# Optimization experiments

Measured on AMD Instinct MI355X. Metric: run time of the kernel, lower is better.

The kernel has to match this reference:

```python
import jax, jax.numpy as jnp
import numpy as np

B, S, D, E = 4, 4096, 1024, 8

def setup_inputs() -> dict:
    key = jax.random.key(0)
    k_h, k_wr, k_br, k_we = jax.random.split(key, 4)
    h = jax.random.normal(k_h, (B, S, D), dtype=jnp.float32)
    # route_weights: nn.Linear(D, E) -> weight [E, D], bias [E]
    W_route = jax.random.normal(k_wr, (E, D), dtype=jnp.float32) / np.sqrt(D)
    b_route = jax.random.normal(k_br, (E,), dtype=jnp.float32) * 0.01
    # edge_transforms: E x nn.Linear(D, D, bias=False) -> stacked [E, D_out, D_in]
    W_edges = jax.random.normal(k_we, (E, D, D), dtype=jnp.float32) / np.sqrt(D)
    layer_bias = jnp.zeros((D,), dtype=jnp.float32)
    return {"h": h, "W_route": W_route, "b_route": b_route,
            "W_edges": W_edges, "layer_bias": layer_bias}

def reference(h, W_route, b_route, W_edges, layer_bias):
    # route_logits = h @ W_route.T + b_route -> [B, S, E]
    route_logits = jnp.einsum('bsd,ed->bse', h, W_route) + b_route
    rw = jax.nn.softmax(route_logits, axis=-1)
    # fused: sum_e rw[b,s,e] * (h @ W_e.T) -> [B, S, D]
    out = jnp.einsum('bsd,efd,bse->bsf', h, W_edges, rw)
    out = out + layer_bias
    return jax.nn.gelu(out, approximate=False)  # torch F.gelu default is exact erf
```

## Files before the change

### kernel.cpp

```cpp
#include <hip/hip_runtime.h>
#include <hip/hip_bf16.h>

#define M_TOK 16384
#define DDIM  1024
#define NEXP  8
#define KP    (NEXP * DDIM)

typedef __bf16 bf16x8 __attribute__((ext_vector_type(8)));
typedef __bf16 bf16x4 __attribute__((ext_vector_type(4)));
typedef float  floatx4 __attribute__((ext_vector_type(4)));

__device__ __forceinline__ void gload_lds16(const void* g, void* l) {
    __builtin_amdgcn_global_load_lds(
        (__attribute__((address_space(1))) void*)(void*)g,
        (__attribute__((address_space(3))) void*)l,
        16, 0, 0);
}

#define CONV_BLOCKS  2048
#define ROUTE_BLOCKS 4096

__global__ __launch_bounds__(256) void prep_kernel(
    const float* __restrict__ h, const float* __restrict__ Wr,
    const float* __restrict__ br, const float* __restrict__ We,
    __bf16* __restrict__ hbf, float* __restrict__ rw, __bf16* __restrict__ Bp)
{
    __shared__ float Wrs[NEXP * DDIM];
    const int tid = threadIdx.x;

    if (blockIdx.x < CONV_BLOCKS) {
        size_t idx = ((size_t)blockIdx.x * 256 + tid) * 16;
        int e = (int)(idx >> 20);
        int f = (int)(idx >> 10) & 1023;
        int k = (int)idx & 1023;
        const float4* s4 = (const float4*)(We + idx);
        float a[16];
        #pragma unroll
        for (int i = 0; i < 4; ++i) {
            float4 v = s4[i];
            a[i*4+0] = v.x; a[i*4+1] = v.y; a[i*4+2] = v.z; a[i*4+3] = v.w;
        }
        bf16x8 o0, o1;
        #pragma unroll
        for (int i = 0; i < 8; ++i) { o0[i] = (__bf16)a[i]; o1[i] = (__bf16)a[8 + i]; }
        __bf16* d = Bp + (size_t)f * KP + (size_t)e * DDIM + k;
        *(bf16x8*)d       = o0;
        *(bf16x8*)(d + 8) = o1;
        return;
    }

    {
        const float4* s4 = (const float4*)Wr;
        float4* d4 = (float4*)Wrs;
        #pragma unroll
        for (int j = 0; j < 8; ++j) d4[j * 256 + tid] = s4[j * 256 + tid];
    }
    __syncthreads();

    const int wave = tid >> 6, lane = tid & 63;
    const int m = (blockIdx.x - CONV_BLOCKS) * 4 + wave;

    const float4* hrow4 = (const float4*)(h + (size_t)m * DDIM);
    float4 a[4];
    #pragma unroll
    for (int j = 0; j < 4; ++j) a[j] = hrow4[j * 64 + lane];

    #pragma unroll
    for (int j = 0; j < 4; ++j) {
        bf16x4 o;
        o[0] = (__bf16)a[j].x; o[1] = (__bf16)a[j].y;
        o[2] = (__bf16)a[j].z; o[3] = (__bf16)a[j].w;
        *(bf16x4*)(hbf + (size_t)m * DDIM + j * 256 + lane * 4) = o;
    }

    const float4* Wrs4 = (const float4*)Wrs;
    float p[NEXP];
    #pragma unroll
    for (int e = 0; e < NEXP; ++e) {
        float s = 0.f;
        #pragma unroll
        for (int j = 0; j < 4; ++j) {
            float4 wv = Wrs4[e * 256 + j * 64 + lane];
            s += a[j].x*wv.x + a[j].y*wv.y + a[j].z*wv.z + a[j].w*wv.w;
        }
        p[e] = s;
    }
    #pragma unroll
    for (int e = 0; e < NEXP; ++e) {
        #pragma unroll
        for (int off = 32; off > 0; off >>= 1)
            p[e] += __shfl_xor(p[e], off, 64);
    }
    if (lane == 0) {
        float l[NEXP], mx = -1e30f;
        #pragma unroll
        for (int e = 0; e < NEXP; ++e) { l[e] = p[e] + br[e]; mx = fmaxf(mx, l[e]); }
        float s = 0.f;
        #pragma unroll
        for (int e = 0; e < NEXP; ++e) { l[e] = expf(l[e] - mx); s += l[e]; }
        float inv = 1.f / s;
        float4 r0 = {l[0]*inv, l[1]*inv, l[2]*inv, l[3]*inv};
        float4 r1 = {l[4]*inv, l[5]*inv, l[6]*inv, l[7]*inv};
        *(float4*)(rw + (size_t)m * NEXP)     = r0;
        *(float4*)(rw + (size_t)m * NEXP + 4) = r1;
    }
}

__global__ __launch_bounds__(512, 2) void gemm_fused_kernel(
    const __bf16* __restrict__ hbf, const __bf16* __restrict__ Bp,
    const float* __restrict__ rw, const float* __restrict__ bias,
    float* __restrict__ outp)
{
    __shared__ __bf16 As[4][256 * 32];
    __shared__ __bf16 Bs[4][256 * 32];

    const int tid  = threadIdx.x;
    const int wave = tid >> 6, lane = tid & 63;
    const int quad = lane >> 4, l16 = lane & 15;
    const int wm = wave >> 2, wn = wave & 3;
    const int m0 = blockIdx.y * 256, f0 = blockIdx.x * 256;

    const int arow = wm * 128 + l16;
    const int brow = wn * 64  + l16;
    const int aoff0 = (arow * 4 + (quad ^ ((arow >> 1) & 3))) * 16;
    const int boff0 = (brow * 4 + (quad ^ ((brow >> 1) & 3))) * 16;

    const int srow = tid >> 2;
    const int scol = ((tid & 3) ^ ((srow >> 1) & 3)) * 8;
    const int aBase = (m0 + srow) * DDIM + scol;
    const int bBase = (f0 + srow) * KP + scol;

    floatx4 facc[8][4];
    const floatx4 z4 = {0.f, 0.f, 0.f, 0.f};
    #pragma unroll
    for (int i = 0; i < 8; ++i)
        #pragma unroll
        for (int j = 0; j < 4; ++j) facc[i][j] = z4;

    {
        const __bf16* a0 = hbf + aBase;
        const __bf16* b0 = Bp  + bBase;
        gload_lds16(a0,                 (char*)&As[0][0] + tid * 16);
        gload_lds16(b0,                 (char*)&Bs[0][0] + tid * 16);
        gload_lds16(a0 + 131072,        (char*)&As[0][0] + tid * 16 + 8192);
        gload_lds16(b0 + 1048576,       (char*)&Bs[0][0] + tid * 16 + 8192);
        gload_lds16(a0 + 32,            (char*)&As[1][0] + tid * 16);
        gload_lds16(b0 + 32,            (char*)&Bs[1][0] + tid * 16);
        gload_lds16(a0 + 131072 + 32,   (char*)&As[1][0] + tid * 16 + 8192);
        gload_lds16(b0 + 1048576 + 32,  (char*)&Bs[1][0] + tid * 16 + 8192);
    }

    #pragma unroll 1
    for (int e = 0; e < NEXP; ++e) {
        if (e > 0) {
            #pragma unroll
            for (int mf = 0; mf < 8; ++mf) {
                #pragma unroll
                for (int r = 0; r < 4; ++r) {
                    int row = m0 + wm * 128 + mf * 16 + quad * 4 + r;
                    float wp = fmaxf(rw[(size_t)row * NEXP + e - 1], 1e-20f);
                    float wc = fmaxf(rw[(size_t)row * NEXP + e],     1e-20f);
                    float ratio = wp / wc;
                    #pragma unroll
                    for (int nf = 0; nf < 4; ++nf) facc[mf][nf][r] *= ratio;
                }
            }
        }
        #pragma unroll 1
        for (int kt4 = 0; kt4 < 8; ++kt4) {
            #pragma unroll
            for (int u = 0; u < 4; ++u) {
                const int t  = (e << 5) + (kt4 << 2) + u;
                const int tt = (t + 2) & 255;
                const __bf16* asrc = hbf + aBase + ((tt & 31) << 5);
                const __bf16* bsrc = Bp  + bBase + (tt << 5);
                char* ad = (char*)&As[(u + 2) & 3][0] + tid * 16;
                char* bd = (char*)&Bs[(u + 2) & 3][0] + tid * 16;
                const char* Ab = (const char*)&As[u][0];
                const char* Bb = (const char*)&Bs[u][0];

                asm volatile("s_waitcnt vmcnt(4)" ::: "memory");
                asm volatile("s_barrier" ::: "memory");

                bf16x8 av0[4], bv[4];
                #pragma unroll
                for (int mf = 0; mf < 4; ++mf)
                    av0[mf] = *(const bf16x8*)(Ab + aoff0 + mf * 1024);
                #pragma unroll
                for (int nf = 0; nf < 4; ++nf)
                    bv[nf] = *(const bf16x8*)(Bb + boff0 + nf * 1024);
                gload_lds16(asrc, ad);
                gload_lds16(bsrc, bd);

                asm volatile("s_barrier" ::: "memory");
                asm volatile("s_waitcnt lgkmcnt(0)" ::: "memory");
                __builtin_amdgcn_sched_barrier(0);
                __builtin_amdgcn_s_setprio(1);
                #pragma unroll
                for (int mf = 0; mf < 4; ++mf)
                    #pragma unroll
                    for (int nf = 0; nf < 4; ++nf)
                        facc[mf][nf] = __builtin_amdgcn_mfma_f32_16x16x32_bf16(
                            av0[mf], bv[nf], facc[mf][nf], 0, 0, 0);
                __builtin_amdgcn_sched_barrier(0);
                __builtin_amdgcn_s_setprio(0);
                asm volatile("s_barrier" ::: "memory");

                bf16x8 av1[4];
                #pragma unroll
                for (int mf = 0; mf < 4; ++mf)
                    av1[mf] = *(const bf16x8*)(Ab + aoff0 + (4 + mf) * 1024);
                gload_lds16(asrc + 131072,  ad + 8192);
                gload_lds16(bsrc + 1048576, bd + 8192);

                asm volatile("s_barrier" ::: "memory");
                asm volatile("s_waitcnt lgkmcnt(0)" ::: "memory");
                __builtin_amdgcn_sched_barrier(0);
                __builtin_amdgcn_s_setprio(1);
                #pragma unroll
                for (int mf = 0; mf < 4; ++mf)
                    #pragma unroll
                    for (int nf = 0; nf < 4; ++nf)
                        facc[4 + mf][nf] = __builtin_amdgcn_mfma_f32_16x16x32_bf16(
                            av1[mf], bv[nf], facc[4 + mf][nf], 0, 0, 0);
                __builtin_amdgcn_sched_barrier(0);
                __builtin_amdgcn_s_setprio(0);
            }
        }
    }

    asm volatile("s_waitcnt vmcnt(0)" ::: "memory");

    float bval[4];
    #pragma unroll
    for (int nf = 0; nf < 4; ++nf) bval[nf] = bias[f0 + wn * 64 + nf * 16 + l16];
    #pragma unroll
    for (int mf = 0; mf < 8; ++mf) {
        #pragma unroll
        for (int r = 0; r < 4; ++r) {
            int gm = m0 + wm * 128 + mf * 16 + quad * 4 + r;
            float w7 = fmaxf(rw[(size_t)gm * NEXP + 7], 1e-20f);
            #pragma unroll
            for (int nf = 0; nf < 4; ++nf) {
                float x = facc[mf][nf][r] * w7 + bval[nf];
                float gel = 0.5f * x * (1.0f + erff(x * 0.70710678118f));
                outp[(size_t)gm * DDIM + (f0 + wn * 64 + nf * 16 + l16)] = gel;
            }
        }
    }
}

extern "C" void kernel_launch(void* const* d_in, const int* in_sizes, int n_in,
                              void* d_out, int out_size, void* d_ws, size_t ws_size,
                              hipStream_t stream) {
    const float* h    = (const float*)d_in[0];
    const float* Wr   = (const float*)d_in[1];
    const float* br   = (const float*)d_in[2];
    const float* We   = (const float*)d_in[3];
    const float* bias = (const float*)d_in[4];
    float* outp = (float*)d_out;
    char* ws = (char*)d_ws;

    __bf16* hbf = (__bf16*)ws;
    __bf16* Bp  = (__bf16*)(ws + (size_t)M_TOK * DDIM * 2);
    float*  rwp = (float*)(ws + (size_t)M_TOK * DDIM * 2
                              + (size_t)NEXP * DDIM * DDIM * 2);

    hipLaunchKernelGGL(prep_kernel, dim3(CONV_BLOCKS + ROUTE_BLOCKS), dim3(256),
                       0, stream, h, Wr, br, We, hbf, rwp, Bp);
    hipLaunchKernelGGL(gemm_fused_kernel, dim3(DDIM / 256, M_TOK / 256),
                       dim3(512), 0, stream, hbf, Bp, rwp, bias, outp);
}
```

Baseline: 437.4 us.

## Remap GEMM blocks to XCDs for B-tile reuse, simplify pipeline, cache routing weights in LDS

The 2D grid becomes a 1D grid of 256 blocks with a swizzle: each XCD pair shares one 256-column slice of the expert weights, so the large weight panel (8192 K) is reused from that XCD's L2. The per-stage pipeline is simplified from two barrier-separated half steps to one barrier per stage, issuing all four async global-to-LDS loads at once before the MFMAs. Routing weights for the block's 256 rows are staged in LDS once instead of being re-read from global memory at each expert rescale and in the epilogue. This relies on the assumed round-robin block-to-XCD dispatch, and fewer barriers may change how LDS reads overlap with MFMA.

```diff
diff --git a/kernel.cpp b/kernel.cpp
--- a/kernel.cpp
+++ b/kernel.cpp
@@ -113,12 +113,19 @@
 {
     __shared__ __bf16 As[4][256 * 32];
     __shared__ __bf16 Bs[4][256 * 32];
+    __shared__ float  rws[256 * NEXP];
 
     const int tid  = threadIdx.x;
     const int wave = tid >> 6, lane = tid & 63;
     const int quad = lane >> 4, l16 = lane & 15;
     const int wm = wave >> 2, wn = wave & 3;
-    const int m0 = blockIdx.y * 256, f0 = blockIdx.x * 256;
+
+    const int L = blockIdx.x;
+    const int xcd = L & 7, slotid = L >> 3;
+    const int f0 = (xcd >> 1) * 256;
+    const int m0 = (((xcd & 1) << 5) + slotid) * 256;
+
+    ((float4*)rws)[tid] = ((const float4*)(rw + (size_t)m0 * NEXP))[tid];
 
     const int arow = wm * 128 + l16;
     const int brow = wn * 64  + l16;
@@ -127,8 +134,8 @@
 
     const int srow = tid >> 2;
     const int scol = ((tid & 3) ^ ((srow >> 1) & 3)) * 8;
-    const int aBase = (m0 + srow) * DDIM + scol;
-    const int bBase = (f0 + srow) * KP + scol;
+    const size_t aBase = (size_t)(m0 + srow) * DDIM + scol;
+    const size_t bBase = (size_t)(f0 + srow) * KP + scol;
 
     floatx4 facc[8][4];
     const floatx4 z4 = {0.f, 0.f, 0.f, 0.f};
@@ -136,6 +143,8 @@
     for (int i = 0; i < 8; ++i)
         #pragma unroll
         for (int j = 0; j < 4; ++j) facc[i][j] = z4;
+
+    __syncthreads();
 
     {
         const __bf16* a0 = hbf + aBase;
@@ -151,81 +160,65 @@
     }
 
     #pragma unroll 1
-    for (int e = 0; e < NEXP; ++e) {
-        if (e > 0) {
+    for (int tb = 0; tb < 64; ++tb) {
+        if (tb && (tb & 7) == 0) {
+            const int e = tb >> 3;
             #pragma unroll
             for (int mf = 0; mf < 8; ++mf) {
                 #pragma unroll
                 for (int r = 0; r < 4; ++r) {
-                    int row = m0 + wm * 128 + mf * 16 + quad * 4 + r;
-                    float wp = fmaxf(rw[(size_t)row * NEXP + e - 1], 1e-20f);
-                    float wc = fmaxf(rw[(size_t)row * NEXP + e],     1e-20f);
+                    int row = wm * 128 + mf * 16 + quad * 4 + r;
+                    float wp = fmaxf(rws[row * NEXP + e - 1], 1e-20f);
+                    float wc = fmaxf(rws[row * NEXP + e],     1e-20f);
                     float ratio = wp / wc;
                     #pragma unroll
                     for (int nf = 0; nf < 4; ++nf) facc[mf][nf][r] *= ratio;
                 }
             }
         }
-        #pragma unroll 1
-        for (int kt4 = 0; kt4 < 8; ++kt4) {
-            #pragma unroll
-            for (int u = 0; u < 4; ++u) {
-                const int t  = (e << 5) + (kt4 << 2) + u;
-                const int tt = (t + 2) & 255;
-                const __bf16* asrc = hbf + aBase + ((tt & 31) << 5);
-                const __bf16* bsrc = Bp  + bBase + (tt << 5);
-                char* ad = (char*)&As[(u + 2) & 3][0] + tid * 16;
-                char* bd = (char*)&Bs[(u + 2) & 3][0] + tid * 16;
-                const char* Ab = (const char*)&As[u][0];
-                const char* Bb = (const char*)&Bs[u][0];
-
-                asm volatile("s_waitcnt vmcnt(4)" ::: "memory");
-                asm volatile("s_barrier" ::: "memory");
-
-                bf16x8 av0[4], bv[4];
-                #pragma unroll
-                for (int mf = 0; mf < 4; ++mf)
-                    av0[mf] = *(const bf16x8*)(Ab + aoff0 + mf * 1024);
+        #pragma unroll
+        for (int u = 0; u < 4; ++u) {
+            const int t  = (tb << 2) + u;
+            const int tt = (t + 2) & 255;
+            const __bf16* asrc = hbf + aBase + (size_t)((tt & 31) << 5);
+            const __bf16* bsrc = Bp  + bBase + ((size_t)tt << 5);
+            char* ad = (char*)&As[(u + 2) & 3][0] + tid * 16;
+            char* bd = (char*)&Bs[(u + 2) & 3][0] + tid * 16;
+            const char* Ab = (const char*)&As[u][0];
+            const char* Bb = (const char*)&Bs[u][0];
+
+            asm volatile("s_waitcnt vmcnt(4)" ::: "memory");
+            asm volatile("s_barrier" ::: "memory");
+
+            gload_lds16(asrc,           ad);
+            gload_lds16(bsrc,           bd);
+            gload_lds16(asrc + 131072,  ad + 8192);
+            gload_lds16(bsrc + 1048576, bd + 8192);
+
+            bf16x8 av0[4], av1[4], bv[4];
+            #pragma unroll
+            for (int nf = 0; nf < 4; ++nf)
+                bv[nf] = *(const bf16x8*)(Bb + boff0 + nf * 1024);
+            #pragma unroll
+            for (int mf = 0; mf < 4; ++mf) {
+                av0[mf] = *(const bf16x8*)(Ab + aoff0 + mf * 1024);
+                av1[mf] = *(const bf16x8*)(Ab + aoff0 + (4 + mf) * 1024);
+            }
+
+            __builtin_amdgcn_s_setprio(1);
+            #pragma unroll
+            for (int mf = 0; mf < 4; ++mf)
                 #pragma unroll
                 for (int nf = 0; nf < 4; ++nf)
-                    bv[nf] = *(const bf16x8*)(Bb + boff0 + nf * 1024);
-                gload_lds16(asrc, ad);
-                gload_lds16(bsrc, bd);
-
-                asm volatile("s_barrier" ::: "memory");
-                asm volatile("s_waitcnt lgkmcnt(0)" ::: "memory");
-                __builtin_amdgcn_sched_barrier(0);
-                __builtin_amdgcn_s_setprio(1);
+                    facc[mf][nf] = __builtin_amdgcn_mfma_f32_16x16x32_bf16(
+                        av0[mf], bv[nf], facc[mf][nf], 0, 0, 0);
+            #pragma unroll
+            for (int mf = 0; mf < 4; ++mf)
                 #pragma unroll
-                for (int mf = 0; mf < 4; ++mf)
-                    #pragma unroll
-                    for (int nf = 0; nf < 4; ++nf)
-                        facc[mf][nf] = __builtin_amdgcn_mfma_f32_16x16x32_bf16(
-                            av0[mf], bv[nf], facc[mf][nf], 0, 0, 0);
-                __builtin_amdgcn_sched_barrier(0);
-                __builtin_amdgcn_s_setprio(0);
-                asm volatile("s_barrier" ::: "memory");
-
-                bf16x8 av1[4];
-                #pragma unroll
-                for (int mf = 0; mf < 4; ++mf)
-                    av1[mf] = *(const bf16x8*)(Ab + aoff0 + (4 + mf) * 1024);
-                gload_lds16(asrc + 131072,  ad + 8192);
-                gload_lds16(bsrc + 1048576, bd + 8192);
-
-                asm volatile("s_barrier" ::: "memory");
-                asm volatile("s_waitcnt lgkmcnt(0)" ::: "memory");
-                __builtin_amdgcn_sched_barrier(0);
-                __builtin_amdgcn_s_setprio(1);
-                #pragma unroll
-                for (int mf = 0; mf < 4; ++mf)
-                    #pragma unroll
-                    for (int nf = 0; nf < 4; ++nf)
-                        facc[4 + mf][nf] = __builtin_amdgcn_mfma_f32_16x16x32_bf16(
-                            av1[mf], bv[nf], facc[4 + mf][nf], 0, 0, 0);
-                __builtin_amdgcn_sched_barrier(0);
-                __builtin_amdgcn_s_setprio(0);
-            }
+                for (int nf = 0; nf < 4; ++nf)
+                    facc[4 + mf][nf] = __builtin_amdgcn_mfma_f32_16x16x32_bf16(
+                        av1[mf], bv[nf], facc[4 + mf][nf], 0, 0, 0);
+            __builtin_amdgcn_s_setprio(0);
         }
     }
 
@@ -238,8 +231,9 @@
     for (int mf = 0; mf < 8; ++mf) {
         #pragma unroll
         for (int r = 0; r < 4; ++r) {
-            int gm = m0 + wm * 128 + mf * 16 + quad * 4 + r;
-            float w7 = fmaxf(rw[(size_t)gm * NEXP + 7], 1e-20f);
+            int lrow = wm * 128 + mf * 16 + quad * 4 + r;
+            int gm = m0 + lrow;
+            float w7 = fmaxf(rws[lrow * NEXP + 7], 1e-20f);
             #pragma unroll
             for (int nf = 0; nf < 4; ++nf) {
                 float x = facc[mf][nf][r] * w7 + bval[nf];
@@ -268,6 +262,6 @@
 
     hipLaunchKernelGGL(prep_kernel, dim3(CONV_BLOCKS + ROUTE_BLOCKS), dim3(256),
                        0, stream, h, Wr, br, We, hbf, rwp, Bp);
-    hipLaunchKernelGGL(gemm_fused_kernel, dim3(DDIM / 256, M_TOK / 256),
-                       dim3(512), 0, stream, hbf, Bp, rwp, bias, outp);
-}
+    hipLaunchKernelGGL(gemm_fused_kernel, dim3(256), dim3(512),
+                       0, stream, hbf, Bp, rwp, bias, outp);
+}
```

After: 413.2 us. -5.5%, faster.
